# Kernel tuning notes

Measured on AMD Instinct MI355X. Metric: run time of the kernel, lower is better.

## Reference

```python
import jax, jax.numpy as jnp
import numpy as np

H = 1024
NH = 16
HD = H // NH
EPS = 1e-5


def setup_inputs() -> dict:
    key = jax.random.key(0)
    ks = jax.random.split(key, 16)
    B, LQ, LK = 2, 1024, 2048
    s = 1.0 / np.sqrt(H)
    inp = {
        "query": jax.random.normal(ks[0], (B, LQ, H), jnp.float32),
        "key": jax.random.normal(ks[1], (B, LK, H), jnp.float32),
        "value": jax.random.normal(ks[2], (B, LK, H), jnp.float32),
        "mask": jax.random.randint(ks[3], (B, LQ, LK), 0, 2, jnp.int32),
        "Wq": jax.random.normal(ks[4], (H, H), jnp.float32) * s,
        "bq": jnp.zeros((H,), jnp.float32),
        "Wk": jax.random.normal(ks[5], (H, H), jnp.float32) * s,
        "bk": jnp.zeros((H,), jnp.float32),
        "Wv": jax.random.normal(ks[6], (H, H), jnp.float32) * s,
        "bv": jnp.zeros((H,), jnp.float32),
        "Wo": jax.random.normal(ks[7], (H, H), jnp.float32) * s,
        "bo": jnp.zeros((H,), jnp.float32),
        "ln_g": jnp.ones((H,), jnp.float32),
        "ln_b": jnp.zeros((H,), jnp.float32),
    }
    return inp


def _split_heads(x, B, L):
    # [B, L, H] -> [B, NH, L, HD]
    return x.reshape(B, L, NH, HD).transpose(0, 2, 1, 3)


def reference(query, key, value, mask, Wq, bq, Wk, bk, Wv, bv, Wo, bo, ln_g, ln_b):
    B, LQ, _ = query.shape
    LK = key.shape[1]
    # projections (torch Linear: x @ W.T + b)
    Q = _split_heads(query @ Wq.T + bq, B, LQ)   # [B,NH,LQ,HD]
    K = _split_heads(key   @ Wk.T + bk, B, LK)   # [B,NH,LK,HD]
    V = _split_heads(value @ Wv.T + bv, B, LK)   # [B,NH,LK,HD]
    scores = jnp.einsum('bhqd,bhkd->bhqk', Q, K) / np.sqrt(HD)
    scores = jnp.where(mask[:, None, :, :] == 0, jnp.float32(-1e9), scores)
    attn = jax.nn.softmax(scores, axis=-1)
    # dropout is identity in eval mode
    ctx = jnp.einsum('bhqk,bhkd->bhqd', attn, V)            # [B,NH,LQ,HD]
    ctx = ctx.transpose(0, 2, 1, 3).reshape(B, LQ, H)       # [B,LQ,H]
    out = ctx @ Wo.T + bo
    x = out + query
    mu = jnp.mean(x, axis=-1, keepdims=True)
    var = jnp.mean(jnp.square(x - mu), axis=-1, keepdims=True)
    return (x - mu) / jnp.sqrt(var + EPS) * ln_g + ln_b
```

## Files before the change

### kernel.cpp

```cpp
#include <hip/hip_runtime.h>
#include <hip/hip_bf16.h>

typedef __hip_bfloat16 hbf16;

#define Hdim 1024
#define NHEAD 16
#define HDIM 64
#define BATCH 2
#define LQ 1024
#define LK 2048
#define LN_EPS 1e-5f

typedef __bf16 bfv8 __attribute__((ext_vector_type(8)));
typedef float floatx4 __attribute__((ext_vector_type(4)));
typedef union { bfv8 v; __bf16 b[8]; unsigned short s[8]; } bfu8;

#define BK 32
#define LDS_PITCH 40
#define QT 64
#define KT 64
#define KS_PITCH 72
#define VT_OFF(d) ((d) * 72 + (((d) >> 3) << 3))
#define PS_OFF(r) ((r) * 72 + (((r) >> 2) << 3))

__device__ inline bfv8 cvt2(const float4 x, const float4 y) {
    bfv8 r = {(__bf16)x.x, (__bf16)x.y, (__bf16)x.z, (__bf16)x.w,
              (__bf16)y.x, (__bf16)y.y, (__bf16)y.z, (__bf16)y.w};
    return r;
}

__device__ __forceinline__ void glds16(const void* g, void* l) {
    __builtin_amdgcn_global_load_lds(
        (const __attribute__((address_space(1))) void*)g,
        (__attribute__((address_space(3))) void*)l, 16, 0, 0);
}

__global__ __launch_bounds__(256) void cvt_all(
    const float* __restrict__ q, const float* __restrict__ k,
    const float* __restrict__ v, const float* __restrict__ Wq,
    const float* __restrict__ Wk, const float* __restrict__ Wv,
    hbf16* __restrict__ qb, hbf16* __restrict__ kb, hbf16* __restrict__ vb,
    hbf16* __restrict__ Wqb, hbf16* __restrict__ Wkb, hbf16* __restrict__ Wvb) {
    const int blk = blockIdx.x;
    const float* src; hbf16* dst; int base;
    if (blk < 1024)      { src = q;  dst = qb;  base = blk; }
    else if (blk < 3072) { src = k;  dst = kb;  base = blk - 1024; }
    else if (blk < 5120) { src = v;  dst = vb;  base = blk - 3072; }
    else if (blk < 5632) { src = Wq; dst = Wqb; base = blk - 5120; }
    else if (blk < 6144) { src = Wk; dst = Wkb; base = blk - 5632; }
    else                 { src = Wv; dst = Wvb; base = blk - 6144; }
    const size_t e = (size_t)base * 2048 + (size_t)threadIdx.x * 8;
    const float4 a = *(const float4*)(src + e);
    const float4 b = *(const float4*)(src + e + 4);
    *(bfv8*)((__bf16*)dst + e) = cvt2(a, b);
}

__global__ __launch_bounds__(256) void proj3_glds(
    const hbf16* __restrict__ qb, const hbf16* __restrict__ kb,
    const hbf16* __restrict__ vb,
    const hbf16* __restrict__ Wqb, const hbf16* __restrict__ Wkb,
    const hbf16* __restrict__ Wvb,
    const float* __restrict__ bq, const float* __restrict__ bk,
    const float* __restrict__ bv,
    hbf16* __restrict__ Qp, hbf16* __restrict__ Kp, hbf16* __restrict__ Vp) {
    const int z = blockIdx.z;
    if (z == 0 && blockIdx.y >= (BATCH * LQ) / 128) return;
    const hbf16* A; const hbf16* W; const float* bias; hbf16* out; float scale;
    if (z == 0)      { A = qb; W = Wqb; bias = bq; out = Qp; scale = 0.125f; }
    else if (z == 1) { A = kb; W = Wkb; bias = bk; out = Kp; scale = 1.0f; }
    else             { A = vb; W = Wvb; bias = bv; out = Vp; scale = 1.0f; }

    __shared__ __align__(16) __bf16 As[128 * 32];
    __shared__ __align__(16) __bf16 Bs[128 * 32];
    const int tid = threadIdx.x;
    const int lane = tid & 63;
    const int w = tid >> 6;
    const int wm = w & 1, wn = w >> 1;
    const int u = lane & 15;
    const int quad = lane >> 4;
    const int rowBase = blockIdx.y * 128;
    const int colBase = blockIdx.x * 128;

    const int srow = tid >> 2;
    const int scol = (tid & 3) * 8;
    const hbf16* aP = A + (size_t)(rowBase + srow) * Hdim + scol;
    const hbf16* wP = W + (size_t)(colBase + srow) * Hdim + scol;
    __bf16* ldsA = &As[srow * 32 + scol];
    __bf16* ldsB = &Bs[srow * 32 + scol];

    floatx4 acc[4][4];
#pragma unroll
    for (int mi = 0; mi < 4; ++mi)
#pragma unroll
        for (int ni = 0; ni < 4; ++ni) acc[mi][ni] = (floatx4){0.f, 0.f, 0.f, 0.f};

    for (int k0 = 0; k0 < Hdim; k0 += 32) {
        __syncthreads();
        glds16(aP + k0, ldsA);
        glds16(aP + k0 + (size_t)64 * Hdim, ldsA + 64 * 32);
        glds16(wP + k0, ldsB);
        glds16(wP + k0 + (size_t)64 * Hdim, ldsB + 64 * 32);
        __syncthreads();

        bfv8 af[4], bf[4];
#pragma unroll
        for (int mi = 0; mi < 4; ++mi)
            af[mi] = *(const bfv8*)&As[(wm * 64 + mi * 16 + u) * 32 + quad * 8];
#pragma unroll
        for (int ni = 0; ni < 4; ++ni)
            bf[ni] = *(const bfv8*)&Bs[(wn * 64 + ni * 16 + u) * 32 + quad * 8];
#pragma unroll
        for (int mi = 0; mi < 4; ++mi)
#pragma unroll
            for (int ni = 0; ni < 4; ++ni)
                acc[mi][ni] = __builtin_amdgcn_mfma_f32_16x16x32_bf16(af[mi], bf[ni], acc[mi][ni], 0, 0, 0);
    }

#pragma unroll
    for (int mi = 0; mi < 4; ++mi)
#pragma unroll
        for (int ni = 0; ni < 4; ++ni) {
            const int n = colBase + wn * 64 + ni * 16 + u;
            const float bn = bias[n];
#pragma unroll
            for (int rr = 0; rr < 4; ++rr) {
                const int m = rowBase + wm * 64 + mi * 16 + quad * 4 + rr;
                out[(size_t)m * Hdim + n] = __float2bfloat16((acc[mi][ni][rr] + bn) * scale);
            }
        }
}

__global__ __launch_bounds__(256) void gemm_ctx_glds(const hbf16* __restrict__ A,
                                                     const float* __restrict__ W,
                                                     const float* __restrict__ bias,
                                                     const float* __restrict__ resid,
                                                     float* __restrict__ out) {
    __shared__ __align__(16) __bf16 As[128 * 32];
    __shared__ __align__(16) __bf16 Bs[128 * 32];
    const int tid = threadIdx.x;
    const int lane = tid & 63;
    const int w = tid >> 6;
    const int wm = w & 1, wn = w >> 1;
    const int u = lane & 15;
    const int quad = lane >> 4;
    const int rowBase = blockIdx.y * 128;
    const int colBase = blockIdx.x * 128;

    const int srow = tid >> 2;
    const int scol = (tid & 3) * 8;
    const hbf16* aP = A + (size_t)(rowBase + srow) * Hdim + scol;
    __bf16* ldsA = &As[srow * 32 + scol];

    const int brow = tid >> 1;
    const int bcol = (tid & 1) * 16;
    const float* wP = W + (size_t)(colBase + brow) * Hdim + bcol;
    __bf16* ldsBw = &Bs[brow * 32 + bcol];

    floatx4 acc[4][4];
#pragma unroll
    for (int mi = 0; mi < 4; ++mi)
#pragma unroll
        for (int ni = 0; ni < 4; ++ni) acc[mi][ni] = (floatx4){0.f, 0.f, 0.f, 0.f};

    for (int k0 = 0; k0 < Hdim; k0 += 32) {
        const float4* w4 = (const float4*)(wP + k0);
        const float4 w0 = w4[0], w1 = w4[1], w2 = w4[2], w3 = w4[3];
        __syncthreads();
        glds16(aP + k0, ldsA);
        glds16(aP + k0 + (size_t)64 * Hdim, ldsA + 64 * 32);
        *(bfv8*)ldsBw = cvt2(w0, w1);
        *(bfv8*)(ldsBw + 8) = cvt2(w2, w3);
        __syncthreads();

        bfv8 af[4], bf[4];
#pragma unroll
        for (int mi = 0; mi < 4; ++mi)
            af[mi] = *(const bfv8*)&As[(wm * 64 + mi * 16 + u) * 32 + quad * 8];
#pragma unroll
        for (int ni = 0; ni < 4; ++ni)
            bf[ni] = *(const bfv8*)&Bs[(wn * 64 + ni * 16 + u) * 32 + quad * 8];
#pragma unroll
        for (int mi = 0; mi < 4; ++mi)
#pragma unroll
            for (int ni = 0; ni < 4; ++ni)
                acc[mi][ni] = __builtin_amdgcn_mfma_f32_16x16x32_bf16(af[mi], bf[ni], acc[mi][ni], 0, 0, 0);
    }

#pragma unroll
    for (int mi = 0; mi < 4; ++mi)
#pragma unroll
        for (int ni = 0; ni < 4; ++ni) {
            const int n = colBase + wn * 64 + ni * 16 + u;
            const float bn = bias[n];
#pragma unroll
            for (int rr = 0; rr < 4; ++rr) {
                const int m = rowBase + wm * 64 + mi * 16 + quad * 4 + rr;
                out[(size_t)m * Hdim + n] = acc[mi][ni][rr] + bn + resid[(size_t)m * Hdim + n];
            }
        }
}

__global__ __launch_bounds__(256) void proj3_mfma(
    const float* __restrict__ q_in, const float* __restrict__ k_in,
    const float* __restrict__ v_in,
    const float* __restrict__ Wq, const float* __restrict__ bq,
    const float* __restrict__ Wk, const float* __restrict__ bk,
    const float* __restrict__ Wv, const float* __restrict__ bv,
    hbf16* __restrict__ Qp, hbf16* __restrict__ Kp, hbf16* __restrict__ Vp) {
    const int z = blockIdx.z;
    if (z == 0 && blockIdx.y >= (BATCH * LQ) / 64) return;
    const float* A; const float* W; const float* bias; hbf16* out; float scale;
    if (z == 0)      { A = q_in; W = Wq; bias = bq; out = Qp; scale = 0.125f; }
    else if (z == 1) { A = k_in; W = Wk; bias = bk; out = Kp; scale = 1.0f; }
    else             { A = v_in; W = Wv; bias = bv; out = Vp; scale = 1.0f; }

    __shared__ __align__(16) __bf16 As[64 * LDS_PITCH];
    __shared__ __align__(16) __bf16 Bs[64 * LDS_PITCH];
    const int tid = threadIdx.x;
    const int lane = tid & 63;
    const int w = tid >> 6;
    const int wm = w & 1, wn = w >> 1;
    const int rowBase = blockIdx.y * 64;
    const int colBase = blockIdx.x * 64;
    const int sr = tid >> 2;
    const int scg = (tid & 3) * 8;
    const int lr = lane & 15;
    const int quad = lane >> 4;

    floatx4 acc[2][2] = {};

    for (int k0 = 0; k0 < Hdim; k0 += BK) {
        const float* ap = A + (size_t)(rowBase + sr) * Hdim + k0 + scg;
        bfv8 av = cvt2(((const float4*)ap)[0], ((const float4*)ap)[1]);
        const float* wp = W + (size_t)(colBase + sr) * Hdim + k0 + scg;
        bfv8 bv8 = cvt2(((const float4*)wp)[0], ((const float4*)wp)[1]);
        __syncthreads();
        *(bfv8*)&As[sr * LDS_PITCH + scg] = av;
        *(bfv8*)&Bs[sr * LDS_PITCH + scg] = bv8;
        __syncthreads();

        bfv8 bf[2];
#pragma unroll
        for (int nt = 0; nt < 2; ++nt)
            bf[nt] = *(const bfv8*)&Bs[(wn * 32 + nt * 16 + lr) * LDS_PITCH + quad * 8];
#pragma unroll
        for (int mt = 0; mt < 2; ++mt) {
            bfv8 af = *(const bfv8*)&As[(wm * 32 + mt * 16 + lr) * LDS_PITCH + quad * 8];
#pragma unroll
            for (int nt = 0; nt < 2; ++nt)
                acc[mt][nt] = __builtin_amdgcn_mfma_f32_16x16x32_bf16(af, bf[nt], acc[mt][nt], 0, 0, 0);
        }
    }

#pragma unroll
    for (int mt = 0; mt < 2; ++mt)
#pragma unroll
        for (int nt = 0; nt < 2; ++nt) {
            const int n = colBase + wn * 32 + nt * 16 + lr;
            const float bn = bias[n];
#pragma unroll
            for (int rr = 0; rr < 4; ++rr) {
                const int m = rowBase + wm * 32 + mt * 16 + quad * 4 + rr;
                out[(size_t)m * Hdim + n] = __float2bfloat16((acc[mt][nt][rr] + bn) * scale);
            }
        }
}

__global__ __launch_bounds__(256) void gemm_mfma_f32(const float* __restrict__ A,
                                                     const float* __restrict__ W,
                                                     const float* __restrict__ bias,
                                                     hbf16* __restrict__ out,
                                                     float scale) {
    __shared__ __align__(16) __bf16 As[64 * LDS_PITCH];
    __shared__ __align__(16) __bf16 Bs[64 * LDS_PITCH];
    const int tid = threadIdx.x;
    const int lane = tid & 63;
    const int w = tid >> 6;
    const int wm = w & 1, wn = w >> 1;
    const int rowBase = blockIdx.y * 64;
    const int colBase = blockIdx.x * 64;
    const int sr = tid >> 2;
    const int scg = (tid & 3) * 8;
    const int lr = lane & 15;
    const int quad = lane >> 4;

    floatx4 acc[2][2] = {};

    for (int k0 = 0; k0 < Hdim; k0 += BK) {
        const float* ap = A + (size_t)(rowBase + sr) * Hdim + k0 + scg;
        bfv8 av = cvt2(((const float4*)ap)[0], ((const float4*)ap)[1]);
        const float* wp = W + (size_t)(colBase + sr) * Hdim + k0 + scg;
        bfv8 bv = cvt2(((const float4*)wp)[0], ((const float4*)wp)[1]);
        __syncthreads();
        *(bfv8*)&As[sr * LDS_PITCH + scg] = av;
        *(bfv8*)&Bs[sr * LDS_PITCH + scg] = bv;
        __syncthreads();

        bfv8 bf[2];
#pragma unroll
        for (int nt = 0; nt < 2; ++nt)
            bf[nt] = *(const bfv8*)&Bs[(wn * 32 + nt * 16 + lr) * LDS_PITCH + quad * 8];
#pragma unroll
        for (int mt = 0; mt < 2; ++mt) {
            bfv8 af = *(const bfv8*)&As[(wm * 32 + mt * 16 + lr) * LDS_PITCH + quad * 8];
#pragma unroll
            for (int nt = 0; nt < 2; ++nt)
                acc[mt][nt] = __builtin_amdgcn_mfma_f32_16x16x32_bf16(af, bf[nt], acc[mt][nt], 0, 0, 0);
        }
    }

#pragma unroll
    for (int mt = 0; mt < 2; ++mt)
#pragma unroll
        for (int nt = 0; nt < 2; ++nt) {
            const int n = colBase + wn * 32 + nt * 16 + lr;
            const float bn = bias[n];
#pragma unroll
            for (int rr = 0; rr < 4; ++rr) {
                const int m = rowBase + wm * 32 + mt * 16 + quad * 4 + rr;
                out[(size_t)m * Hdim + n] = __float2bfloat16((acc[mt][nt][rr] + bn) * scale);
            }
        }
}

__global__ __launch_bounds__(256) void gemm_mfma_ctx(const hbf16* __restrict__ A,
                                                     const float* __restrict__ W,
                                                     const float* __restrict__ bias,
                                                     const float* __restrict__ resid,
                                                     float* __restrict__ out) {
    __shared__ __align__(16) __bf16 As[64 * LDS_PITCH];
    __shared__ __align__(16) __bf16 Bs[64 * LDS_PITCH];
    const int tid = threadIdx.x;
    const int lane = tid & 63;
    const int w = tid >> 6;
    const int wm = w & 1, wn = w >> 1;
    const int rowBase = blockIdx.y * 64;
    const int colBase = blockIdx.x * 64;
    const int sr = tid >> 2;
    const int scg = (tid & 3) * 8;
    const int lr = lane & 15;
    const int quad = lane >> 4;

    floatx4 acc[2][2] = {};

    for (int k0 = 0; k0 < Hdim; k0 += BK) {
        bfv8 av = *(const bfv8*)(A + (size_t)(rowBase + sr) * Hdim + k0 + scg);
        const float* wp = W + (size_t)(colBase + sr) * Hdim + k0 + scg;
        bfv8 bv = cvt2(((const float4*)wp)[0], ((const float4*)wp)[1]);
        __syncthreads();
        *(bfv8*)&As[sr * LDS_PITCH + scg] = av;
        *(bfv8*)&Bs[sr * LDS_PITCH + scg] = bv;
        __syncthreads();

        bfv8 bf[2];
#pragma unroll
        for (int nt = 0; nt < 2; ++nt)
            bf[nt] = *(const bfv8*)&Bs[(wn * 32 + nt * 16 + lr) * LDS_PITCH + quad * 8];
#pragma unroll
        for (int mt = 0; mt < 2; ++mt) {
            bfv8 af = *(const bfv8*)&As[(wm * 32 + mt * 16 + lr) * LDS_PITCH + quad * 8];
#pragma unroll
            for (int nt = 0; nt < 2; ++nt)
                acc[mt][nt] = __builtin_amdgcn_mfma_f32_16x16x32_bf16(af, bf[nt], acc[mt][nt], 0, 0, 0);
        }
    }

#pragma unroll
    for (int mt = 0; mt < 2; ++mt)
#pragma unroll
        for (int nt = 0; nt < 2; ++nt) {
            const int n = colBase + wn * 32 + nt * 16 + lr;
            const float bn = bias[n];
#pragma unroll
            for (int rr = 0; rr < 4; ++rr) {
                const int m = rowBase + wm * 32 + mt * 16 + quad * 4 + rr;
                out[(size_t)m * Hdim + n] = acc[mt][nt][rr] + bn + resid[(size_t)m * Hdim + n];
            }
        }
}

__global__ __launch_bounds__(256) void mask_prep_st(const int* __restrict__ mask,
                                                    hbf16* __restrict__ mbias) {
    const int t = blockIdx.x;
    const int kt = t & 31;
    const int qb = (t >> 5) & 15;
    const int b = t >> 9;
    const int tid = threadIdx.x;
    const int w = tid >> 6;
    const int lane = tid & 63;
    const int quad = lane >> 4;
    const int u = lane & 15;
    const int qrow = qb * 64 + w * 16 + quad * 4;
    const int kcol = kt * 64 + u;
    const int* mp = mask + ((size_t)(b * LQ + qrow)) * LK + kcol;

    bfu8 v0, v1;
#pragma unroll
    for (int ns = 0; ns < 4; ++ns)
#pragma unroll
        for (int rr = 0; rr < 4; ++rr) {
            const int mv = mp[(size_t)rr * LK + ns * 16];
            const __bf16 bias = (mv == 0) ? (__bf16)(-1e9f) : (__bf16)(-10.0f);
            const int j = ns * 4 + rr;
            if (j < 8) v0.b[j] = bias; else v1.b[j - 8] = bias;
        }
    __bf16* dst = (__bf16*)mbias + (size_t)t * 4096 + tid * 16;
    *(bfv8*)dst = v0.v;
    *(bfv8*)(dst + 8) = v1.v;
}

__global__ __launch_bounds__(256, 4) void attn_split(const hbf16* __restrict__ Qp,
                                                     const hbf16* __restrict__ Kp,
                                                     const hbf16* __restrict__ Vp,
                                                     const hbf16* __restrict__ mbias,
                                                     float* __restrict__ Opart,
                                                     float* __restrict__ lpart) {
    const int qb = blockIdx.x;
    const int h = blockIdx.y;
    const int b = blockIdx.z >> 1;
    const int sp = blockIdx.z & 1;
    const int tid = threadIdx.x;
    const int lane = tid & 63;
    const int w = tid >> 6;
    const int u = lane & 15;
    const int quad = lane >> 4;
    const int qBase = qb * QT;

    __shared__ __align__(16) __bf16 Ks[64 * KS_PITCH];
    __shared__ __align__(16) __bf16 Vt[4672];
    __shared__ __align__(16) __bf16 Ps[4][1184];

    const int qrow_frag = qBase + w * 16 + u;
    const hbf16* qptr = Qp + (size_t)(b * LQ + qrow_frag) * Hdim + h * HDIM + quad * 8;
    const bfv8 af_q0 = *(const bfv8*)qptr;
    const bfv8 af_q1 = *(const bfv8*)(qptr + 32);

    float l_acc[4] = {0.f, 0.f, 0.f, 0.f};
    floatx4 acc_o[4];
#pragma unroll
    for (int nd = 0; nd < 4; ++nd) acc_o[nd] = (floatx4){0.f, 0.f, 0.f, 0.f};

    const int sk = tid >> 2;
    const int sdg = (tid & 3) * 16;
    const int vk2 = (tid >> 3) * 2;
    const int vd0 = (tid & 7) * 8;
    const __bf16* mbT = (const __bf16*)mbias + (size_t)(b * 16 + qb) * 32 * 4096 + tid * 16;

    const int kt0 = sp * (LK / KT / 2);
    for (int kt = kt0; kt < kt0 + (LK / KT / 2); ++kt) {
        const int kBase = kt * KT;

        bfu8 mb0, mb1;
        mb0.v = *(const bfv8*)(mbT + (size_t)kt * 4096);
        mb1.v = *(const bfv8*)(mbT + (size_t)kt * 4096 + 8);

        const hbf16* vp0 = Vp + (size_t)(b * LK + kBase + vk2) * Hdim + h * HDIM + vd0;
        bfu8 v0, v1;
        v0.v = *(const bfv8*)vp0;
        v1.v = *(const bfv8*)(vp0 + Hdim);
        const hbf16* kp = Kp + (size_t)(b * LK + kBase + sk) * Hdim + h * HDIM + sdg;
        const bfv8 kv0 = *(const bfv8*)kp;
        const bfv8 kv1 = *(const bfv8*)(kp + 8);

        __syncthreads();
        *(bfv8*)&Ks[sk * KS_PITCH + sdg] = kv0;
        *(bfv8*)&Ks[sk * KS_PITCH + sdg + 8] = kv1;
#pragma unroll
        for (int i = 0; i < 8; ++i) {
            unsigned int pk = (unsigned int)v0.s[i] | ((unsigned int)v1.s[i] << 16);
            *(unsigned int*)&Vt[VT_OFF(vd0 + i) + vk2] = pk;
        }
        __syncthreads();

        floatx4 acc_s[4];
#pragma unroll
        for (int ns = 0; ns < 4; ++ns) {
            const bfv8 bk0 = *(const bfv8*)&Ks[(ns * 16 + u) * KS_PITCH + quad * 8];
            const bfv8 bk1 = *(const bfv8*)&Ks[(ns * 16 + u) * KS_PITCH + quad * 8 + 32];
            floatx4 a = (floatx4){0.f, 0.f, 0.f, 0.f};
            a = __builtin_amdgcn_mfma_f32_16x16x32_bf16(af_q0, bk0, a, 0, 0, 0);
            a = __builtin_amdgcn_mfma_f32_16x16x32_bf16(af_q1, bk1, a, 0, 0, 0);
            acc_s[ns] = a;
        }

        __bf16* Pw = Ps[w];
#pragma unroll
        for (int ns = 0; ns < 4; ++ns)
#pragma unroll
            for (int rr = 0; rr < 4; ++rr) {
                const int j = ns * 4 + rr;
                const float bias = (j < 8) ? (float)mb0.b[j] : (float)mb1.b[j - 8];
                const float p = __expf(acc_s[ns][rr] + bias);
                Pw[PS_OFF(quad * 4 + rr) + ns * 16 + u] = (__bf16)p;
                l_acc[rr] += p;
            }

        const bfv8 af_p0 = *(const bfv8*)&Pw[PS_OFF(u) + quad * 8];
        const bfv8 af_p1 = *(const bfv8*)&Pw[PS_OFF(u) + quad * 8 + 32];
#pragma unroll
        for (int nd = 0; nd < 4; ++nd) {
            const bfv8 bv0 = *(const bfv8*)&Vt[VT_OFF(nd * 16 + u) + quad * 8];
            const bfv8 bv1 = *(const bfv8*)&Vt[VT_OFF(nd * 16 + u) + quad * 8 + 32];
            acc_o[nd] = __builtin_amdgcn_mfma_f32_16x16x32_bf16(af_p0, bv0, acc_o[nd], 0, 0, 0);
            acc_o[nd] = __builtin_amdgcn_mfma_f32_16x16x32_bf16(af_p1, bv1, acc_o[nd], 0, 0, 0);
        }
    }

#pragma unroll
    for (int rr = 0; rr < 4; ++rr) {
        float l = l_acc[rr];
        l += __shfl_xor(l, 1, 64);
        l += __shfl_xor(l, 2, 64);
        l += __shfl_xor(l, 4, 64);
        l += __shfl_xor(l, 8, 64);
        const int qrow = qBase + w * 16 + quad * 4 + rr;
        const size_t m = (size_t)(b * LQ + qrow);
        float* orow = Opart + (size_t)sp * (BATCH * LQ * Hdim) + m * Hdim + h * HDIM;
#pragma unroll
        for (int nd = 0; nd < 4; ++nd)
            orow[nd * 16 + u] = acc_o[nd][rr];
        if (u == 0)
            lpart[(size_t)sp * (BATCH * LQ * NHEAD) + m * NHEAD + h] = l;
    }
}

__global__ __launch_bounds__(256) void merge_ctx(const float* __restrict__ Opart,
                                                 const float* __restrict__ lpart,
                                                 hbf16* __restrict__ ctx) {
    const size_t m = blockIdx.x;
    const int t = threadIdx.x;
    const int kk = t * 4;
    const int h = kk >> 6;
    const float l = lpart[m * NHEAD + h] +
                    lpart[(size_t)(BATCH * LQ * NHEAD) + m * NHEAD + h];
    const float invl = 1.0f / l;
    const float4 a = ((const float4*)(Opart + m * Hdim))[t];
    const float4 c = ((const float4*)(Opart + (size_t)(BATCH * LQ * Hdim) + m * Hdim))[t];
    hbf16* crow = ctx + m * Hdim + kk;
    crow[0] = __float2bfloat16((a.x + c.x) * invl);
    crow[1] = __float2bfloat16((a.y + c.y) * invl);
    crow[2] = __float2bfloat16((a.z + c.z) * invl);
    crow[3] = __float2bfloat16((a.w + c.w) * invl);
}

__global__ __launch_bounds__(256, 4) void attn_flash_st(const hbf16* __restrict__ Qp,
                                                        const hbf16* __restrict__ Kp,
                                                        const hbf16* __restrict__ Vp,
                                                        const hbf16* __restrict__ mbias,
                                                        hbf16* __restrict__ ctx) {
    const int qb = blockIdx.x;
    const int h = blockIdx.y;
    const int b = blockIdx.z;
    const int tid = threadIdx.x;
    const int lane = tid & 63;
    const int w = tid >> 6;
    const int u = lane & 15;
    const int quad = lane >> 4;
    const int qBase = qb * QT;

    __shared__ __align__(16) __bf16 Ks[64 * KS_PITCH];
    __shared__ __align__(16) __bf16 Vt[4672];
    __shared__ __align__(16) __bf16 Ps[4][1184];

    const int qrow_frag = qBase + w * 16 + u;
    const hbf16* qptr = Qp + (size_t)(b * LQ + qrow_frag) * Hdim + h * HDIM + quad * 8;
    const bfv8 af_q0 = *(const bfv8*)qptr;
    const bfv8 af_q1 = *(const bfv8*)(qptr + 32);

    float l_acc[4] = {0.f, 0.f, 0.f, 0.f};
    floatx4 acc_o[4];
#pragma unroll
    for (int nd = 0; nd < 4; ++nd) acc_o[nd] = (floatx4){0.f, 0.f, 0.f, 0.f};

    const int sk = tid >> 2;
    const int sdg = (tid & 3) * 16;
    const int vk2 = (tid >> 3) * 2;
    const int vd0 = (tid & 7) * 8;
    const __bf16* mbT = (const __bf16*)mbias + (size_t)(b * 16 + qb) * 32 * 4096 + tid * 16;

    for (int kt = 0; kt < LK / KT; ++kt) {
        const int kBase = kt * KT;

        bfu8 mb0, mb1;
        mb0.v = *(const bfv8*)(mbT + (size_t)kt * 4096);
        mb1.v = *(const bfv8*)(mbT + (size_t)kt * 4096 + 8);

        const hbf16* vp0 = Vp + (size_t)(b * LK + kBase + vk2) * Hdim + h * HDIM + vd0;
        bfu8 v0, v1;
        v0.v = *(const bfv8*)vp0;
        v1.v = *(const bfv8*)(vp0 + Hdim);
        const hbf16* kp = Kp + (size_t)(b * LK + kBase + sk) * Hdim + h * HDIM + sdg;
        const bfv8 kv0 = *(const bfv8*)kp;
        const bfv8 kv1 = *(const bfv8*)(kp + 8);

        __syncthreads();
        *(bfv8*)&Ks[sk * KS_PITCH + sdg] = kv0;
        *(bfv8*)&Ks[sk * KS_PITCH + sdg + 8] = kv1;
#pragma unroll
        for (int i = 0; i < 8; ++i) {
            unsigned int pk = (unsigned int)v0.s[i] | ((unsigned int)v1.s[i] << 16);
            *(unsigned int*)&Vt[VT_OFF(vd0 + i) + vk2] = pk;
        }
        __syncthreads();

        floatx4 acc_s[4];
#pragma unroll
        for (int ns = 0; ns < 4; ++ns) {
            const bfv8 bk0 = *(const bfv8*)&Ks[(ns * 16 + u) * KS_PITCH + quad * 8];
            const bfv8 bk1 = *(const bfv8*)&Ks[(ns * 16 + u) * KS_PITCH + quad * 8 + 32];
            floatx4 a = (floatx4){0.f, 0.f, 0.f, 0.f};
            a = __builtin_amdgcn_mfma_f32_16x16x32_bf16(af_q0, bk0, a, 0, 0, 0);
            a = __builtin_amdgcn_mfma_f32_16x16x32_bf16(af_q1, bk1, a, 0, 0, 0);
            acc_s[ns] = a;
        }

        __bf16* Pw = Ps[w];
#pragma unroll
        for (int ns = 0; ns < 4; ++ns)
#pragma unroll
            for (int rr = 0; rr < 4; ++rr) {
                const int j = ns * 4 + rr;
                const float bias = (j < 8) ? (float)mb0.b[j] : (float)mb1.b[j - 8];
                const float p = __expf(acc_s[ns][rr] + bias);
                Pw[PS_OFF(quad * 4 + rr) + ns * 16 + u] = (__bf16)p;
                l_acc[rr] += p;
            }

        const bfv8 af_p0 = *(const bfv8*)&Pw[PS_OFF(u) + quad * 8];
        const bfv8 af_p1 = *(const bfv8*)&Pw[PS_OFF(u) + quad * 8 + 32];
#pragma unroll
        for (int nd = 0; nd < 4; ++nd) {
            const bfv8 bv0 = *(const bfv8*)&Vt[VT_OFF(nd * 16 + u) + quad * 8];
            const bfv8 bv1 = *(const bfv8*)&Vt[VT_OFF(nd * 16 + u) + quad * 8 + 32];
            acc_o[nd] = __builtin_amdgcn_mfma_f32_16x16x32_bf16(af_p0, bv0, acc_o[nd], 0, 0, 0);
            acc_o[nd] = __builtin_amdgcn_mfma_f32_16x16x32_bf16(af_p1, bv1, acc_o[nd], 0, 0, 0);
        }
    }

#pragma unroll
    for (int rr = 0; rr < 4; ++rr) {
        float l = l_acc[rr];
        l += __shfl_xor(l, 1, 64);
        l += __shfl_xor(l, 2, 64);
        l += __shfl_xor(l, 4, 64);
        l += __shfl_xor(l, 8, 64);
        const float invl = 1.0f / l;
        const int qrow = qBase + w * 16 + quad * 4 + rr;
        hbf16* crow = ctx + (size_t)(b * LQ + qrow) * Hdim + h * HDIM;
#pragma unroll
        for (int nd = 0; nd < 4; ++nd)
            crow[nd * 16 + u] = __float2bfloat16(acc_o[nd][rr] * invl);
    }
}

__global__ __launch_bounds__(256) void ln_kernel(float* __restrict__ x,
                                                 const float* __restrict__ g,
                                                 const float* __restrict__ beta) {
    const int row = blockIdx.x;
    float* xr = x + (size_t)row * Hdim;
    __shared__ float red[256];
    const int tid = threadIdx.x;

    const float4 xi = ((const float4*)xr)[tid];
    red[tid] = xi.x + xi.y + xi.z + xi.w;
    __syncthreads();
    for (int st = 128; st > 0; st >>= 1) {
        if (tid < st) red[tid] += red[tid + st];
        __syncthreads();
    }
    const float mu = red[0] * (1.0f / Hdim);
    __syncthreads();
    {
        float dx = xi.x - mu, dy = xi.y - mu, dz = xi.z - mu, dw = xi.w - mu;
        red[tid] = dx * dx + dy * dy + dz * dz + dw * dw;
    }
    __syncthreads();
    for (int st = 128; st > 0; st >>= 1) {
        if (tid < st) red[tid] += red[tid + st];
        __syncthreads();
    }
    const float rstd = rsqrtf(red[0] * (1.0f / Hdim) + LN_EPS);

    const float4 g4 = ((const float4*)g)[tid];
    const float4 b4 = ((const float4*)beta)[tid];
    float4 y;
    y.x = (xi.x - mu) * rstd * g4.x + b4.x;
    y.y = (xi.y - mu) * rstd * g4.y + b4.y;
    y.z = (xi.z - mu) * rstd * g4.z + b4.z;
    y.w = (xi.w - mu) * rstd * g4.w + b4.w;
    ((float4*)xr)[tid] = y;
}

__device__ inline float wave_red_sum(float v) {
    v += __shfl_down(v, 32, 64);
    v += __shfl_down(v, 16, 64);
    v += __shfl_down(v, 8, 64);
    v += __shfl_down(v, 4, 64);
    v += __shfl_down(v, 2, 64);
    v += __shfl_down(v, 1, 64);
    return v;
}

__global__ __launch_bounds__(256) void fused_mha(
    const float* __restrict__ q_in, const float* __restrict__ k_in,
    const float* __restrict__ v_in, const int* __restrict__ mask,
    const float* __restrict__ Wq, const float* __restrict__ bq,
    const float* __restrict__ Wk, const float* __restrict__ bk,
    const float* __restrict__ Wv, const float* __restrict__ bv,
    const float* __restrict__ Wo, const float* __restrict__ bo,
    const float* __restrict__ ln_g, const float* __restrict__ ln_b,
    float* __restrict__ out) {
    const int q = blockIdx.x;
    const int b = blockIdx.y;
    const int tid = threadIdx.x;
    const int lane = tid & 63;
    const int w = tid >> 6;

    __shared__ float qrow[Hdim];
    __shared__ float qt[Hdim];
    __shared__ float sc[LK];
    __shared__ float u[Hdim];
    __shared__ float ctxv[Hdim];
    __shared__ float Qh[HDIM];
    __shared__ float red[256];
    __shared__ float sb_sh;

    const float* qp = q_in + (size_t)(b * LQ + q) * Hdim;
    for (int i = tid; i < Hdim; i += 256) qrow[i] = qp[i];
    __syncthreads();

    const float* keyb = k_in + (size_t)b * LK * Hdim;
    const float* valb = v_in + (size_t)b * LK * Hdim;
    const int* mrow = mask + (size_t)(b * LQ + q) * LK;

    for (int h = 0; h < NHEAD; ++h) {
        for (int dd = w; dd < HDIM; dd += 4) {
            const float4* wrow = (const float4*)(Wq + (size_t)(h * HDIM + dd) * Hdim);
            const float4* q4 = (const float4*)qrow;
            float p = 0.f;
#pragma unroll
            for (int i0 = 0; i0 < 4; ++i0) {
                float4 a = wrow[i0 * 64 + lane];
                float4 c = q4[i0 * 64 + lane];
                p += a.x * c.x + a.y * c.y + a.z * c.z + a.w * c.w;
            }
            p = wave_red_sum(p);
            if (lane == 0) Qh[dd] = p + bq[h * HDIM + dd];
        }
        __syncthreads();

        if (tid < HDIM) red[tid] = Qh[tid] * bk[h * HDIM + tid];

        float4 s4 = {0.f, 0.f, 0.f, 0.f};
        for (int d = 0; d < HDIM; ++d) {
            float4 a = ((const float4*)(Wk + (size_t)(h * HDIM + d) * Hdim))[tid];
            float qd = Qh[d];
            s4.x += a.x * qd;
            s4.y += a.y * qd;
            s4.z += a.z * qd;
            s4.w += a.w * qd;
        }
        __syncthreads();
        if (tid == 0) {
            float s = 0.f;
            for (int i = 0; i < HDIM; ++i) s += red[i];
            sb_sh = s;
        }
        ((float4*)qt)[tid] = s4;
        __syncthreads();
        const float sb = sb_sh;

        for (int k = w; k < LK; k += 4) {
            const float4* krow = (const float4*)(keyb + (size_t)k * Hdim);
            const float4* q4 = (const float4*)qt;
            float p = 0.f;
#pragma unroll
            for (int i0 = 0; i0 < 4; ++i0) {
                float4 a = krow[i0 * 64 + lane];
                float4 c = q4[i0 * 64 + lane];
                p += a.x * c.x + a.y * c.y + a.z * c.z + a.w * c.w;
            }
            p = wave_red_sum(p);
            if (lane == 0) {
                float s = (p + sb) * 0.125f;
                if (mrow[k] == 0) s = -1e9f;
                sc[k] = s;
            }
        }
        __syncthreads();

        float m = -1e30f;
        for (int k = tid; k < LK; k += 256) m = fmaxf(m, sc[k]);
        red[tid] = m;
        __syncthreads();
        for (int s = 128; s > 0; s >>= 1) {
            if (tid < s) red[tid] = fmaxf(red[tid], red[tid + s]);
            __syncthreads();
        }
        const float mx = red[0];
        __syncthreads();
        float sum = 0.f;
        for (int k = tid; k < LK; k += 256) {
            float e = __expf(sc[k] - mx);
            sc[k] = e;
            sum += e;
        }
        red[tid] = sum;
        __syncthreads();
        for (int s = 128; s > 0; s >>= 1) {
            if (tid < s) red[tid] += red[tid + s];
            __syncthreads();
        }
        const float inv = 1.0f / red[0];
        for (int k = tid; k < LK; k += 256) sc[k] *= inv;
        __syncthreads();

        {
            float4 acc = {0.f, 0.f, 0.f, 0.f};
            const float4* vb4 = (const float4*)valb;
#pragma unroll 4
            for (int k = 0; k < LK; ++k) {
                float p = sc[k];
                float4 a = vb4[(size_t)k * (Hdim / 4) + tid];
                acc.x += a.x * p;
                acc.y += a.y * p;
                acc.z += a.z * p;
                acc.w += a.w * p;
            }
            ((float4*)u)[tid] = acc;
        }
        __syncthreads();

        for (int dd = w; dd < HDIM; dd += 4) {
            const float4* wrow = (const float4*)(Wv + (size_t)(h * HDIM + dd) * Hdim);
            const float4* u4 = (const float4*)u;
            float p = 0.f;
#pragma unroll
            for (int i0 = 0; i0 < 4; ++i0) {
                float4 a = wrow[i0 * 64 + lane];
                float4 c = u4[i0 * 64 + lane];
                p += a.x * c.x + a.y * c.y + a.z * c.z + a.w * c.w;
            }
            p = wave_red_sum(p);
            if (lane == 0) ctxv[h * HDIM + dd] = p + bv[h * HDIM + dd];
        }
        __syncthreads();
    }

    for (int n = w; n < Hdim; n += 4) {
        const float4* wrow = (const float4*)(Wo + (size_t)n * Hdim);
        const float4* c4 = (const float4*)ctxv;
        float p = 0.f;
#pragma unroll
        for (int i0 = 0; i0 < 4; ++i0) {
            float4 a = wrow[i0 * 64 + lane];
            float4 c = c4[i0 * 64 + lane];
            p += a.x * c.x + a.y * c.y + a.z * c.z + a.w * c.w;
        }
        p = wave_red_sum(p);
        if (lane == 0) qt[n] = p + bo[n] + qrow[n];
    }
    __syncthreads();

    {
        const float4 x4 = ((const float4*)qt)[tid];
        red[tid] = x4.x + x4.y + x4.z + x4.w;
    }
    __syncthreads();
    for (int s = 128; s > 0; s >>= 1) {
        if (tid < s) red[tid] += red[tid + s];
        __syncthreads();
    }
    const float mu = red[0] * (1.0f / Hdim);
    __syncthreads();
    {
        const float4 x4 = ((const float4*)qt)[tid];
        float dx = x4.x - mu, dy = x4.y - mu, dz = x4.z - mu, dw = x4.w - mu;
        red[tid] = dx * dx + dy * dy + dz * dz + dw * dw;
    }
    __syncthreads();
    for (int s = 128; s > 0; s >>= 1) {
        if (tid < s) red[tid] += red[tid + s];
        __syncthreads();
    }
    const float rstd = rsqrtf(red[0] * (1.0f / Hdim) + LN_EPS);

    float* orow = out + (size_t)(b * LQ + q) * Hdim;
    const float4 x4 = ((const float4*)qt)[tid];
    const float4 g4 = ((const float4*)ln_g)[tid];
    const float4 b4 = ((const float4*)ln_b)[tid];
    float4 y;
    y.x = (x4.x - mu) * rstd * g4.x + b4.x;
    y.y = (x4.y - mu) * rstd * g4.y + b4.y;
    y.z = (x4.z - mu) * rstd * g4.z + b4.z;
    y.w = (x4.w - mu) * rstd * g4.w + b4.w;
    ((float4*)orow)[tid] = y;
}

extern "C" void kernel_launch(void* const* d_in, const int* in_sizes, int n_in,
                              void* d_out, int out_size, void* d_ws, size_t ws_size,
                              hipStream_t stream) {
    const float* query = (const float*)d_in[0];
    const float* key   = (const float*)d_in[1];
    const float* value = (const float*)d_in[2];
    const int*   mask  = (const int*)d_in[3];
    const float* Wq = (const float*)d_in[4];
    const float* bq = (const float*)d_in[5];
    const float* Wk = (const float*)d_in[6];
    const float* bk = (const float*)d_in[7];
    const float* Wv = (const float*)d_in[8];
    const float* bv = (const float*)d_in[9];
    const float* Wo = (const float*)d_in[10];
    const float* bo = (const float*)d_in[11];
    const float* ln_g = (const float*)d_in[12];
    const float* ln_b = (const float*)d_in[13];
    float* out = (float*)d_out;

    const size_t MB = 1024 * 1024;
    dim3 blk(256);

    if (ws_size >= 50 * MB) {
        char* p = (char*)d_ws;
        hbf16* Qp    = (hbf16*)(p + 0 * MB);
        hbf16* Kp    = (hbf16*)(p + 4 * MB);
        hbf16* Vp    = (hbf16*)(p + 12 * MB);
        hbf16* ctxb  = (hbf16*)(p + 20 * MB);
        hbf16* mbias = (hbf16*)(p + 24 * MB);
        float* Opart = (float*)(p + 32 * MB);
        float* lpart = (float*)(p + 48 * MB);

        hbf16* qb  = (hbf16*)(p + 20 * MB);
        hbf16* kb  = (hbf16*)(p + 24 * MB);
        hbf16* vb  = (hbf16*)(p + 32 * MB);
        hbf16* Wqb = (hbf16*)(p + 40 * MB);
        hbf16* Wkb = (hbf16*)(p + 42 * MB);
        hbf16* Wvb = (hbf16*)(p + 44 * MB);

        cvt_all<<<dim3(6656), blk, 0, stream>>>(query, key, value, Wq, Wk, Wv,
                                                qb, kb, vb, Wqb, Wkb, Wvb);
        proj3_glds<<<dim3(Hdim / 128, (BATCH * LK) / 128, 3), blk, 0, stream>>>(
            qb, kb, vb, Wqb, Wkb, Wvb, bq, bk, bv, Qp, Kp, Vp);
        mask_prep_st<<<dim3(1024), blk, 0, stream>>>(mask, mbias);

        attn_split<<<dim3(LQ / QT, NHEAD, BATCH * 2), blk, 0, stream>>>(
            Qp, Kp, Vp, mbias, Opart, lpart);
        merge_ctx<<<dim3(BATCH * LQ), blk, 0, stream>>>(Opart, lpart, ctxb);

        gemm_ctx_glds<<<dim3(Hdim / 128, (BATCH * LQ) / 128), blk, 0, stream>>>(
            ctxb, Wo, bo, query, out);
        ln_kernel<<<BATCH * LQ, blk, 0, stream>>>(out, ln_g, ln_b);
    } else if (ws_size >= 32 * MB) {
        char* p = (char*)d_ws;
        hbf16* Qp = (hbf16*)p;    p += 4 * MB;
        hbf16* Kp = (hbf16*)p;    p += 8 * MB;
        hbf16* Vp = (hbf16*)p;    p += 8 * MB;
        hbf16* ctxb = (hbf16*)p;  p += 4 * MB;
        hbf16* mbias = (hbf16*)p; p += 8 * MB;

        gemm_mfma_f32<<<dim3(Hdim / 64, (BATCH * LQ) / 64), blk, 0, stream>>>(query, Wq, bq, Qp, 0.125f);
        gemm_mfma_f32<<<dim3(Hdim / 64, (BATCH * LK) / 64), blk, 0, stream>>>(key, Wk, bk, Kp, 1.0f);
        gemm_mfma_f32<<<dim3(Hdim / 64, (BATCH * LK) / 64), blk, 0, stream>>>(value, Wv, bv, Vp, 1.0f);
        mask_prep_st<<<dim3(1024), blk, 0, stream>>>(mask, mbias);
        attn_flash_st<<<dim3(LQ / QT, NHEAD, BATCH), blk, 0, stream>>>(Qp, Kp, Vp, mbias, ctxb);
        gemm_mfma_ctx<<<dim3(Hdim / 64, (BATCH * LQ) / 64), blk, 0, stream>>>(ctxb, Wo, bo, query, out);
        ln_kernel<<<BATCH * LQ, blk, 0, stream>>>(out, ln_g, ln_b);
    } else {
        fused_mha<<<dim3(LQ, BATCH), dim3(256), 0, stream>>>(
            query, key, value, mask, Wq, bq, Wk, bk, Wv, bv, Wo, bo, ln_g, ln_b, out);
    }
}
```

Baseline: 261.5 us.

## Double-buffer LDS in projection GEMM and retile output GEMM to 64x64

The QKV projection GEMM gains two LDS buffers, so global-to-LDS loads for the next K-slice are issued before the MFMA work on the current slice, with one barrier per step instead of two. The output-projection GEMM moves to 64x64 tiles, launching four times as many blocks to fill the GPU (the old grid had only 128 blocks). It is also double-buffered, with the fp32 Wo slice prefetched into registers and converted to bf16 after compute. The trade-off is more LDS per block in the projection kernel and less data reuse per block in the smaller-tile output GEMM.

```diff
diff --git a/kernel.cpp b/kernel.cpp
--- a/kernel.cpp
+++ b/kernel.cpp
@@ -70,8 +70,8 @@
     else if (z == 1) { A = kb; W = Wkb; bias = bk; out = Kp; scale = 1.0f; }
     else             { A = vb; W = Wvb; bias = bv; out = Vp; scale = 1.0f; }
 
-    __shared__ __align__(16) __bf16 As[128 * 32];
-    __shared__ __align__(16) __bf16 Bs[128 * 32];
+    __shared__ __align__(16) __bf16 As[2][128 * 32];
+    __shared__ __align__(16) __bf16 Bs[2][128 * 32];
     const int tid = threadIdx.x;
     const int lane = tid & 63;
     const int w = tid >> 6;
@@ -85,8 +85,15 @@
     const int scol = (tid & 3) * 8;
     const hbf16* aP = A + (size_t)(rowBase + srow) * Hdim + scol;
     const hbf16* wP = W + (size_t)(colBase + srow) * Hdim + scol;
-    __bf16* ldsA = &As[srow * 32 + scol];
-    __bf16* ldsB = &Bs[srow * 32 + scol];
+    const int ldsOff = srow * 32 + scol;
+
+#define P_STAGE(buf, k0)                                            \
+    do {                                                            \
+        glds16(aP + (k0), &As[buf][ldsOff]);                        \
+        glds16(aP + (k0) + (size_t)64 * Hdim, &As[buf][ldsOff + 64 * 32]); \
+        glds16(wP + (k0), &Bs[buf][ldsOff]);                        \
+        glds16(wP + (k0) + (size_t)64 * Hdim, &Bs[buf][ldsOff + 64 * 32]); \
+    } while (0)
 
     floatx4 acc[4][4];
 #pragma unroll
@@ -94,27 +101,31 @@
 #pragma unroll
         for (int ni = 0; ni < 4; ++ni) acc[mi][ni] = (floatx4){0.f, 0.f, 0.f, 0.f};
 
-    for (int k0 = 0; k0 < Hdim; k0 += 32) {
-        __syncthreads();
-        glds16(aP + k0, ldsA);
-        glds16(aP + k0 + (size_t)64 * Hdim, ldsA + 64 * 32);
-        glds16(wP + k0, ldsB);
-        glds16(wP + k0 + (size_t)64 * Hdim, ldsB + 64 * 32);
-        __syncthreads();
-
-        bfv8 af[4], bf[4];
-#pragma unroll
-        for (int mi = 0; mi < 4; ++mi)
-            af[mi] = *(const bfv8*)&As[(wm * 64 + mi * 16 + u) * 32 + quad * 8];
-#pragma unroll
-        for (int ni = 0; ni < 4; ++ni)
-            bf[ni] = *(const bfv8*)&Bs[(wn * 64 + ni * 16 + u) * 32 + quad * 8];
-#pragma unroll
-        for (int mi = 0; mi < 4; ++mi)
-#pragma unroll
-            for (int ni = 0; ni < 4; ++ni)
-                acc[mi][ni] = __builtin_amdgcn_mfma_f32_16x16x32_bf16(af[mi], bf[ni], acc[mi][ni], 0, 0, 0);
-    }
+#define P_COMPUTE(buf)                                                         \
+    do {                                                                       \
+        bfv8 af[4], bf[4];                                                     \
+        _Pragma("unroll") for (int mi = 0; mi < 4; ++mi)                       \
+            af[mi] = *(const bfv8*)&As[buf][(wm * 64 + mi * 16 + u) * 32 + quad * 8]; \
+        _Pragma("unroll") for (int ni = 0; ni < 4; ++ni)                       \
+            bf[ni] = *(const bfv8*)&Bs[buf][(wn * 64 + ni * 16 + u) * 32 + quad * 8]; \
+        _Pragma("unroll") for (int mi = 0; mi < 4; ++mi)                       \
+            _Pragma("unroll") for (int ni = 0; ni < 4; ++ni)                   \
+                acc[mi][ni] = __builtin_amdgcn_mfma_f32_16x16x32_bf16(af[mi], bf[ni], acc[mi][ni], 0, 0, 0); \
+    } while (0)
+
+    P_STAGE(0, 0);
+    __syncthreads();
+
+    for (int t = 0; t < 32; t += 2) {
+        if (t + 1 < 32) P_STAGE(1, (t + 1) * 32);
+        P_COMPUTE(0);
+        __syncthreads();
+        if (t + 2 < 32) P_STAGE(0, (t + 2) * 32);
+        P_COMPUTE(1);
+        __syncthreads();
+    }
+#undef P_STAGE
+#undef P_COMPUTE
 
 #pragma unroll
     for (int mi = 0; mi < 4; ++mi)
@@ -130,71 +141,97 @@
         }
 }
 
-__global__ __launch_bounds__(256) void gemm_ctx_glds(const hbf16* __restrict__ A,
-                                                     const float* __restrict__ W,
-                                                     const float* __restrict__ bias,
-                                                     const float* __restrict__ resid,
-                                                     float* __restrict__ out) {
-    __shared__ __align__(16) __bf16 As[128 * 32];
-    __shared__ __align__(16) __bf16 Bs[128 * 32];
+__global__ __launch_bounds__(256) void gemm_ctx2(const hbf16* __restrict__ A,
+                                                 const float* __restrict__ W,
+                                                 const float* __restrict__ bias,
+                                                 const float* __restrict__ resid,
+                                                 float* __restrict__ out) {
+    __shared__ __align__(16) __bf16 As[2][64 * 32];
+    __shared__ __align__(16) __bf16 Bs[2][64 * 32];
     const int tid = threadIdx.x;
     const int lane = tid & 63;
     const int w = tid >> 6;
     const int wm = w & 1, wn = w >> 1;
     const int u = lane & 15;
     const int quad = lane >> 4;
-    const int rowBase = blockIdx.y * 128;
-    const int colBase = blockIdx.x * 128;
+    const int rowBase = blockIdx.y * 64;
+    const int colBase = blockIdx.x * 64;
 
     const int srow = tid >> 2;
     const int scol = (tid & 3) * 8;
     const hbf16* aP = A + (size_t)(rowBase + srow) * Hdim + scol;
-    __bf16* ldsA = &As[srow * 32 + scol];
-
-    const int brow = tid >> 1;
-    const int bcol = (tid & 1) * 16;
-    const float* wP = W + (size_t)(colBase + brow) * Hdim + bcol;
-    __bf16* ldsBw = &Bs[brow * 32 + bcol];
-
-    floatx4 acc[4][4];
-#pragma unroll
-    for (int mi = 0; mi < 4; ++mi)
-#pragma unroll
-        for (int ni = 0; ni < 4; ++ni) acc[mi][ni] = (floatx4){0.f, 0.f, 0.f, 0.f};
-
-    for (int k0 = 0; k0 < Hdim; k0 += 32) {
-        const float4* w4 = (const float4*)(wP + k0);
-        const float4 w0 = w4[0], w1 = w4[1], w2 = w4[2], w3 = w4[3];
-        __syncthreads();
-        glds16(aP + k0, ldsA);
-        glds16(aP + k0 + (size_t)64 * Hdim, ldsA + 64 * 32);
-        *(bfv8*)ldsBw = cvt2(w0, w1);
-        *(bfv8*)(ldsBw + 8) = cvt2(w2, w3);
-        __syncthreads();
-
-        bfv8 af[4], bf[4];
-#pragma unroll
-        for (int mi = 0; mi < 4; ++mi)
-            af[mi] = *(const bfv8*)&As[(wm * 64 + mi * 16 + u) * 32 + quad * 8];
-#pragma unroll
-        for (int ni = 0; ni < 4; ++ni)
-            bf[ni] = *(const bfv8*)&Bs[(wn * 64 + ni * 16 + u) * 32 + quad * 8];
-#pragma unroll
-        for (int mi = 0; mi < 4; ++mi)
-#pragma unroll
-            for (int ni = 0; ni < 4; ++ni)
-                acc[mi][ni] = __builtin_amdgcn_mfma_f32_16x16x32_bf16(af[mi], bf[ni], acc[mi][ni], 0, 0, 0);
-    }
-
-#pragma unroll
-    for (int mi = 0; mi < 4; ++mi)
-#pragma unroll
-        for (int ni = 0; ni < 4; ++ni) {
-            const int n = colBase + wn * 64 + ni * 16 + u;
+    const int ldsOffA = srow * 32 + scol;
+
+    const float* wP = W + (size_t)(colBase + srow) * Hdim + scol;
+    const int ldsOffB = ldsOffA;
+
+    floatx4 acc[2][2];
+#pragma unroll
+    for (int mi = 0; mi < 2; ++mi)
+#pragma unroll
+        for (int ni = 0; ni < 2; ++ni) acc[mi][ni] = (floatx4){0.f, 0.f, 0.f, 0.f};
+
+#define C_COMPUTE(buf)                                                         \
+    do {                                                                       \
+        bfv8 af[2], bf[2];                                                     \
+        _Pragma("unroll") for (int mi = 0; mi < 2; ++mi)                       \
+            af[mi] = *(const bfv8*)&As[buf][(wm * 32 + mi * 16 + u) * 32 + quad * 8]; \
+        _Pragma("unroll") for (int ni = 0; ni < 2; ++ni)                       \
+            bf[ni] = *(const bfv8*)&Bs[buf][(wn * 32 + ni * 16 + u) * 32 + quad * 8]; \
+        _Pragma("unroll") for (int mi = 0; mi < 2; ++mi)                       \
+            _Pragma("unroll") for (int ni = 0; ni < 2; ++ni)                   \
+                acc[mi][ni] = __builtin_amdgcn_mfma_f32_16x16x32_bf16(af[mi], bf[ni], acc[mi][ni], 0, 0, 0); \
+    } while (0)
+
+    {
+        glds16(aP, &As[0][ldsOffA]);
+        const float4* w4 = (const float4*)wP;
+        const float4 w0 = w4[0], w1 = w4[1];
+        *(bfv8*)&Bs[0][ldsOffB] = cvt2(w0, w1);
+    }
+    __syncthreads();
+
+    for (int t = 0; t < 32; t += 2) {
+        {
+            float4 w0, w1;
+            const bool pf = (t + 1 < 32);
+            if (pf) {
+                glds16(aP + (t + 1) * 32, &As[1][ldsOffA]);
+                const float4* w4 = (const float4*)(wP + (t + 1) * 32);
+                w0 = w4[0]; w1 = w4[1];
+            }
+            C_COMPUTE(0);
+            if (pf) {
+                *(bfv8*)&Bs[1][ldsOffB] = cvt2(w0, w1);
+            }
+            __syncthreads();
+        }
+        {
+            float4 w0, w1;
+            const bool pf = (t + 2 < 32);
+            if (pf) {
+                glds16(aP + (t + 2) * 32, &As[0][ldsOffA]);
+                const float4* w4 = (const float4*)(wP + (t + 2) * 32);
+                w0 = w4[0]; w1 = w4[1];
+            }
+            C_COMPUTE(1);
+            if (pf) {
+                *(bfv8*)&Bs[0][ldsOffB] = cvt2(w0, w1);
+            }
+            __syncthreads();
+        }
+    }
+#undef C_COMPUTE
+
+#pragma unroll
+    for (int mi = 0; mi < 2; ++mi)
+#pragma unroll
+        for (int ni = 0; ni < 2; ++ni) {
+            const int n = colBase + wn * 32 + ni * 16 + u;
             const float bn = bias[n];
 #pragma unroll
             for (int rr = 0; rr < 4; ++rr) {
-                const int m = rowBase + wm * 64 + mi * 16 + quad * 4 + rr;
+                const int m = rowBase + wm * 32 + mi * 16 + quad * 4 + rr;
                 out[(size_t)m * Hdim + n] = acc[mi][ni][rr] + bn + resid[(size_t)m * Hdim + n];
             }
         }
@@ -946,7 +983,7 @@
             Qp, Kp, Vp, mbias, Opart, lpart);
         merge_ctx<<<dim3(BATCH * LQ), blk, 0, stream>>>(Opart, lpart, ctxb);
 
-        gemm_ctx_glds<<<dim3(Hdim / 128, (BATCH * LQ) / 128), blk, 0, stream>>>(
+        gemm_ctx2<<<dim3(Hdim / 64, (BATCH * LQ) / 64), blk, 0, stream>>>(
             ctxb, Wo, bo, query, out);
         ln_kernel<<<BATCH * LQ, blk, 0, stream>>>(out, ln_g, ln_b);
     } else if (ws_size >= 32 * MB) {
```

After: 246.8 us. 1.06x faster.
